# Performance work log

Measured on AMD Instinct MI355X. Metric: run time of the kernel, lower is better.

The kernel has to match this reference:

```python
import jax, jax.numpy as jnp
import numpy as np

D_MODEL = 2048
D_HEAD = 128
NUM_HEADS = 16
D_KV_LATENT = 512
BATCH = 2
SEQ = 2048


def setup_inputs() -> dict:
    key = jax.random.key(0)
    ks = jax.random.split(key, 6)
    s = 0.02
    return {
        "x": jax.random.normal(ks[0], (BATCH, SEQ, D_MODEL), jnp.float32),
        "Wd": jax.random.normal(ks[1], (D_KV_LATENT, D_MODEL), jnp.float32) * s,
        "Wuk": jax.random.normal(ks[2], (NUM_HEADS * D_HEAD, D_KV_LATENT), jnp.float32) * s,
        "Wuv": jax.random.normal(ks[3], (NUM_HEADS * D_HEAD, D_KV_LATENT), jnp.float32) * s,
        "Wq": jax.random.normal(ks[4], (NUM_HEADS * D_HEAD, D_MODEL), jnp.float32) * s,
        "Wo": jax.random.normal(ks[5], (D_MODEL, NUM_HEADS * D_HEAD), jnp.float32) * s,
        "use_cache": 1,
    }


def _mla_cache_path(x, Wd, Wuk, Wuv, Wq, Wo):
    # Weight-absorbed MLA prefill from an empty cache (total_seq_len == seq_len).
    b, s, dm = x.shape
    h, dh, c = NUM_HEADS, D_HEAD, D_KV_LATENT
    # latents = downsample(x): [b, s, c]
    latents = jnp.einsum("bsm,cm->bsc", x, Wd)
    # absorbed weights: q_uk [h, dm, c], out_uv [h, dm, c]
    q_uk = jnp.einsum("hdm,hdc->hmc", Wq.reshape(h, dh, dm), Wuk.reshape(h, dh, c))
    out_uv = jnp.einsum("mhd,hdc->hmc", Wo.reshape(dm, h, dh), Wuv.reshape(h, dh, c))
    # query_part: [b, h, s, c]
    query_part = jnp.einsum("bsm,hmc->bhsc", x, q_uk)
    # value_part: [b, h, s, dm]
    value_part = jnp.einsum("hmc,btc->bhtm", out_uv, latents)
    # scores over latent dim: [b, h, s, s]
    scores = jnp.einsum("bhsc,btc->bhst", query_part, latents) / np.sqrt(dh).astype(np.float32)
    causal = jnp.triu(jnp.ones((s, s), dtype=bool), k=1)
    scores = jnp.where(causal, -jnp.inf, scores)
    attn = jax.nn.softmax(scores, axis=-1)
    # output already in model dim; sum contributions over heads
    out = jnp.einsum("bhst,bhtm->bsm", attn, value_part)
    return out


def reference(x, Wd, Wuk, Wuv, Wq, Wo, use_cache):
    # use_cache is a static Python int (1 -> weight-absorbed cache path)
    return _mla_cache_path(x, Wd, Wuk, Wuv, Wq, Wo)
```

## Files before the change

### kernel.cpp

```cpp
#include <hip/hip_runtime.h>
#include <hip/hip_bf16.h>

typedef __attribute__((ext_vector_type(8))) short short8x;
typedef __attribute__((ext_vector_type(4))) float f32x4;

__device__ __forceinline__ ushort f2bf(float f){
  union { __hip_bfloat16 b; ushort u; } cvt;
  cvt.b = __float2bfloat16(f);
  return cvt.u;
}

__global__ __launch_bounds__(256) void cvt_kernel(const float* __restrict__ in, ushort* __restrict__ out,
                                                  long n, float scale){
  long i = ((long)blockIdx.x * 256 + threadIdx.x) * 4;
  if (i >= n) return;
  float4 v = *(const float4*)(in + i);
  ushort4 o;
  o.x = f2bf(v.x * scale); o.y = f2bf(v.y * scale); o.z = f2bf(v.z * scale); o.w = f2bf(v.w * scale);
  *(ushort4*)(out + i) = o;
}

template<int OUTBF>
__global__ __launch_bounds__(256, 3)
void gemm_bt(const ushort* __restrict__ A, const ushort* __restrict__ BT, void* __restrict__ Cv,
             int M, int N, int K, int lda, int ldb, int ldc,
             long aZ, long bZ, long cZ, float scale)
{
  __shared__ __align__(16) ushort As[2][128 * 32];
  __shared__ __align__(16) ushort Bs[2][128 * 32];
  const int z = blockIdx.z;
  const ushort* Ab = A + (long)z * aZ;
  const ushort* Bb = BT + (long)z * bZ;
  const int tid = threadIdx.x, lane = tid & 63, w = tid >> 6;
  const int wm = w >> 1, wn = w & 1;
  const int lq = lane & 15, q4 = lane >> 4;

  int lin = blockIdx.x + gridDim.x * blockIdx.y;
  const int cpx = (gridDim.x * gridDim.y) >> 3;
  lin = (lin & 7) * cpx + (lin >> 3);
  const int bx = lin % gridDim.x, by = lin / gridDim.x;

  const long arow = (long)by * 128, brow = (long)bx * 128;
  const int lr = lane >> 2, lc = (lane & 3) * 8;

  const f32x4 z4 = {0.f, 0.f, 0.f, 0.f};
  f32x4 acc[4][4];
#pragma unroll
  for (int i = 0; i < 4; i++)
#pragma unroll
    for (int j = 0; j < 4; j++) acc[i][j] = z4;

  auto stage = [&](int buf, int k0){
#pragma unroll
    for (int is = 0; is < 2; ++is){
      const int rb = is * 64 + w * 16;
      const ushort* ga = Ab + (arow + rb + lr) * (long)lda + k0 + lc;
      const ushort* gb = Bb + (brow + rb + lr) * (long)ldb + k0 + lc;
      __builtin_amdgcn_global_load_lds((const __attribute__((address_space(1))) void*)ga,
                                       (__attribute__((address_space(3))) void*)&As[buf][rb * 32], 16, 0, 0);
      __builtin_amdgcn_global_load_lds((const __attribute__((address_space(1))) void*)gb,
                                       (__attribute__((address_space(3))) void*)&Bs[buf][rb * 32], 16, 0, 0);
    }
  };

  const int nk = K >> 5;
  stage(0, 0);
  for (int kt = 0; kt < nk; ++kt){
    __syncthreads();
    if (kt + 1 < nk) stage((kt + 1) & 1, (kt + 1) * 32);
    const int buf = kt & 1;
    short8x a[4], b[4];
#pragma unroll
    for (int i = 0; i < 4; i++){
      a[i] = *(const short8x*)&As[buf][(wm * 64 + i * 16 + lq) * 32 + q4 * 8];
      b[i] = *(const short8x*)&Bs[buf][(wn * 64 + i * 16 + lq) * 32 + q4 * 8];
    }
#pragma unroll
    for (int i = 0; i < 4; i++)
#pragma unroll
      for (int j = 0; j < 4; j++)
        acc[i][j] = __builtin_amdgcn_mfma_f32_16x16x32_bf16(a[i], b[j], acc[i][j], 0, 0, 0);
  }

  const long crowb = arow + wm * 64;
  const long ccolb = brow + wn * 64;
#pragma unroll
  for (int i = 0; i < 4; i++)
#pragma unroll
    for (int j = 0; j < 4; j++)
#pragma unroll
      for (int r = 0; r < 4; r++){
        const long row = crowb + i * 16 + q4 * 4 + r;
        const long col = ccolb + j * 16 + lq;
        const float v = acc[i][j][r] * scale;
        if (OUTBF) ((ushort*)Cv)[(long)z * cZ + row * ldc + col] = f2bf(v);
        else       ((float*)Cv)[(long)z * cZ + row * ldc + col] = v;
      }
}

__global__ __launch_bounds__(256, 1)
void flash12_kernel(const ushort* __restrict__ q, const ushort* __restrict__ k,
                    const ushort* __restrict__ vT, ushort* __restrict__ attnO)
{
  __shared__ __align__(16) ushort Kb[2][64 * 128];
  __shared__ __align__(16) ushort Vb[2][128 * 64];
  __shared__ __align__(16) ushort Pl[4][2][16][64];

  const int tid = threadIdx.x, lane = tid & 63, w = tid >> 6;
  const int lq = lane & 15, q4 = lane >> 4;

  const int i = blockIdx.x;
  const int pr = i >> 8;
  const int ii = i & 255;
  const int xcd = ii & 7;
  const int bh = xcd * 4 + ((ii >> 3) & 3);
  const int j = ii >> 5;
  const int strip = pr ? j : (15 - j);
  const int b = bh & 1, h = bh >> 1;

  const int nt = 2 * (strip + 1);
  const int wdiag = strip * 2 + (w >> 1);
  const int moff = (w & 1) * 32;

  const ushort* kb_ = k + (long)b * 2048 * 2048 + h * 128;
  const ushort* vb_ = vT + (long)h * 128 * 4096 + (long)b * 2048;

  const int krow0 = w * 4 + (lane >> 4);
  const int kg = (lane & 15) ^ (krow0 & 7);
  const ushort* kbase = kb_ + (long)krow0 * 2048 + kg * 8;
  const int kofs0 = w * 512;

  const int drow0 = w * 8 + (lane >> 3);
  const int vg = (lane & 7) ^ (drow0 & 7);
  const ushort* vbase = vb_ + (long)drow0 * 4096 + vg * 8;
  const int vofs0 = w * 512;

  auto stage = [&](int buf, int tt){
    const ushort* kp = kbase + (long)tt * 64 * 2048;
    const ushort* vp = vbase + (long)tt * 64;
#pragma unroll
    for (int is = 0; is < 4; ++is){
      __builtin_amdgcn_global_load_lds((const __attribute__((address_space(1))) void*)(kp + (long)is * 16 * 2048),
          (__attribute__((address_space(3))) void*)&Kb[buf][kofs0 + is * 2048], 16, 0, 0);
      __builtin_amdgcn_global_load_lds((const __attribute__((address_space(1))) void*)(vp + (long)is * 32 * 4096),
          (__attribute__((address_space(3))) void*)&Vb[buf][vofs0 + is * 2048], 16, 0, 0);
    }
  };

  const f32x4 z4 = {0.f, 0.f, 0.f, 0.f};

  const int qrow0 = strip * 128 + w * 32;
  const long qgbase = (long)b * 2048 + qrow0;

  short8x qf[2][4];
#pragma unroll
  for (int si = 0; si < 2; si++){
    const ushort* qp = q + (qgbase + si * 16 + lq) * 2560 + h * 128 + q4 * 8;
#pragma unroll
    for (int ks = 0; ks < 4; ks++) qf[si][ks] = *(const short8x*)(qp + ks * 32);
  }

  f32x4 oacc[8][2];
#pragma unroll
  for (int dt = 0; dt < 8; dt++){ oacc[dt][0] = z4; oacc[dt][1] = z4; }
  float dsum[2] = {0.f, 0.f};

  const int prx = lq & 7;

  stage(0, 0);
  stage(1, 1);

#pragma unroll 1
  for (int tt = 0; tt < nt; ++tt){
    if (tt == nt - 1) asm volatile("s_waitcnt vmcnt(0)" ::: "memory");
    else              asm volatile("s_waitcnt vmcnt(8)" ::: "memory");
    __syncthreads();
    const int cur = tt & 1;

    if (tt <= wdiag){
      const bool diag = (tt == wdiag);
#pragma unroll
      for (int ti = 0; ti < 4; ++ti){
        const int r = ti * 16 + lq;
        const int rb = r * 128;
        const int rx = r & 7;
        const short8x a0 = *(const short8x*)&Kb[cur][rb + (((q4) ^ rx) * 8)];
        const short8x a1 = *(const short8x*)&Kb[cur][rb + (((4 + q4) ^ rx) * 8)];
        const short8x a2 = *(const short8x*)&Kb[cur][rb + (((8 + q4) ^ rx) * 8)];
        const short8x a3 = *(const short8x*)&Kb[cur][rb + (((12 + q4) ^ rx) * 8)];
        const int cG = (ti * 2 + (q4 >> 1)) ^ prx;
        const int pco = cG * 8 + (q4 & 1) * 4;
#pragma unroll
        for (int si = 0; si < 2; ++si){
          f32x4 st = __builtin_amdgcn_mfma_f32_16x16x32_bf16(a0, qf[si][0], z4, 0, 0, 0);
          st = __builtin_amdgcn_mfma_f32_16x16x32_bf16(a1, qf[si][1], st, 0, 0, 0);
          st = __builtin_amdgcn_mfma_f32_16x16x32_bf16(a2, qf[si][2], st, 0, 0, 0);
          st = __builtin_amdgcn_mfma_f32_16x16x32_bf16(a3, qf[si][3], st, 0, 0, 0);
          ushort4 pb;
#pragma unroll
          for (int r4 = 0; r4 < 4; ++r4){
            const int tl = ti * 16 + q4 * 4 + r4;
            float p = exp2f(st[r4]);
            if (diag && tl > moff + si * 16 + lq) p = 0.f;
            dsum[si] += p;
            ((ushort*)&pb)[r4] = f2bf(p);
          }
          *(ushort4*)&Pl[w][si][lq][pco] = pb;
        }
      }
      asm volatile("s_waitcnt lgkmcnt(0)" ::: "memory");
      __builtin_amdgcn_sched_barrier(0);
      const short8x pf00 = *(const short8x*)&Pl[w][0][lq][(q4 ^ prx) * 8];
      const short8x pf01 = *(const short8x*)&Pl[w][0][lq][((4 + q4) ^ prx) * 8];
      const short8x pf10 = *(const short8x*)&Pl[w][1][lq][(q4 ^ prx) * 8];
      const short8x pf11 = *(const short8x*)&Pl[w][1][lq][((4 + q4) ^ prx) * 8];
      __builtin_amdgcn_sched_barrier(0);
#pragma unroll
      for (int dt = 0; dt < 8; ++dt){
        const int r = dt * 16 + lq;
        const int rb = r * 64;
        const int rx = lq & 7;
        const short8x av0 = *(const short8x*)&Vb[cur][rb + (((q4) ^ rx) * 8)];
        const short8x av1 = *(const short8x*)&Vb[cur][rb + (((4 + q4) ^ rx) * 8)];
        oacc[dt][0] = __builtin_amdgcn_mfma_f32_16x16x32_bf16(av0, pf00, oacc[dt][0], 0, 0, 0);
        oacc[dt][0] = __builtin_amdgcn_mfma_f32_16x16x32_bf16(av1, pf01, oacc[dt][0], 0, 0, 0);
        oacc[dt][1] = __builtin_amdgcn_mfma_f32_16x16x32_bf16(av0, pf10, oacc[dt][1], 0, 0, 0);
        oacc[dt][1] = __builtin_amdgcn_mfma_f32_16x16x32_bf16(av1, pf11, oacc[dt][1], 0, 0, 0);
      }
    }
    __syncthreads();
    if (tt + 2 < nt) stage(cur, tt + 2);
  }

  float inv[2];
#pragma unroll
  for (int si = 0; si < 2; ++si){
    float d = dsum[si];
    d += __shfl_xor(d, 16);
    d += __shfl_xor(d, 32);
    inv[si] = 1.f / d;
  }

#pragma unroll
  for (int dt = 0; dt < 8; dt++)
#pragma unroll
    for (int si = 0; si < 2; si++){
      ushort4 o;
      o.x = f2bf(oacc[dt][si][0] * inv[si]);
      o.y = f2bf(oacc[dt][si][1] * inv[si]);
      o.z = f2bf(oacc[dt][si][2] * inv[si]);
      o.w = f2bf(oacc[dt][si][3] * inv[si]);
      *(ushort4*)(attnO + (qgbase + si * 16 + lq) * 2048 + h * 128 + dt * 16 + q4 * 4) = o;
    }
}

extern "C" void kernel_launch(void* const* d_in, const int* in_sizes, int n_in,
                              void* d_out, int out_size, void* d_ws, size_t ws_size,
                              hipStream_t stream)
{
  const float* x   = (const float*)d_in[0];
  const float* Wd  = (const float*)d_in[1];
  const float* Wuk = (const float*)d_in[2];
  const float* Wuv = (const float*)d_in[3];
  const float* Wq  = (const float*)d_in[4];
  const float* Wo  = (const float*)d_in[5];
  float* out = (float*)d_out;
  ushort* ws = (ushort*)d_ws;

  ushort* xb    = ws + 0L;
  ushort* wqdb  = ws + 8388608L;
  ushort* wob   = ws + 13631488L;
  ushort* wukb  = ws + 17825792L;
  ushort* wuvb  = ws + 18874368L;
  ushort* qlat  = ws + 19922944L;
  ushort* kb    = ws + 30408704L;
  ushort* vTb   = ws + 38797312L;
  ushort* attnO = ws + 47185920L;

  const float QSCL = 0.12751744800f;

  cvt_kernel<<<8192, 256, 0, stream>>>(x,   xb,            8388608L, 1.0f);
  cvt_kernel<<<4096, 256, 0, stream>>>(Wq,  wqdb,          4194304L, QSCL);
  cvt_kernel<<<1024, 256, 0, stream>>>(Wd,  wqdb + 4194304L, 1048576L, 1.0f);
  cvt_kernel<<<4096, 256, 0, stream>>>(Wo,  wob,           4194304L, 1.0f);
  cvt_kernel<<<1024, 256, 0, stream>>>(Wuk, wukb,          1048576L, 1.0f);
  cvt_kernel<<<1024, 256, 0, stream>>>(Wuv, wuvb,          1048576L, 1.0f);

  gemm_bt<1><<<dim3(20, 32, 1), 256, 0, stream>>>(xb, wqdb, qlat, 4096, 2560, 2048,
      2048, 2048, 2560, 0L, 0L, 0L, 1.0f);
  gemm_bt<1><<<dim3(16, 32, 1), 256, 0, stream>>>(qlat + 2048, wukb, kb, 4096, 2048, 512,
      2560, 512, 2048, 0L, 0L, 0L, 1.0f);
  gemm_bt<1><<<dim3(32, 16, 1), 256, 0, stream>>>(wuvb, qlat + 2048, vTb, 2048, 4096, 512,
      512, 2560, 4096, 0L, 0L, 0L, 1.0f);
  flash12_kernel<<<512, 256, 0, stream>>>(qlat, kb, vTb, attnO);
  gemm_bt<0><<<dim3(16, 32, 1), 256, 0, stream>>>(attnO, wob, out, 4096, 2048, 2048,
      2048, 2048, 2048, 0L, 0L, 0L, 1.0f);
}
```

Before: 237.8 us.

## Merge conversion kernels, deepen GEMM prefetch, and shrink flash attention tiles

Merges the six fp32-to-bf16 conversion launches into one kernel that picks its source by index range, which removes launch overhead. The GEMM now prefetches two K-tiles ahead, waits on an explicit vmcnt and allows 4 blocks per CU. The attention kernel moves to 128-thread blocks with 64-row query strips and 32-key tiles, doubling the grid to 1024 blocks for better load balance and occupancy. The P buffer drops its swizzle in favour of padding, and the V reads use a new swizzle. Smaller tiles raise sync and stage overhead per unit of work, and the higher GEMM occupancy may cause register spills.

```diff
diff --git a/kernel.cpp b/kernel.cpp
--- a/kernel.cpp
+++ b/kernel.cpp
@@ -10,18 +10,26 @@
   return cvt.u;
 }
 
-__global__ __launch_bounds__(256) void cvt_kernel(const float* __restrict__ in, ushort* __restrict__ out,
-                                                  long n, float scale){
-  long i = ((long)blockIdx.x * 256 + threadIdx.x) * 4;
-  if (i >= n) return;
-  float4 v = *(const float4*)(in + i);
+__global__ __launch_bounds__(256)
+void cvt_all(const float* __restrict__ x, const float* __restrict__ Wq, const float* __restrict__ Wd,
+             const float* __restrict__ Wo, const float* __restrict__ Wuk, const float* __restrict__ Wuv,
+             ushort* __restrict__ out, float qscl){
+  const long i = ((long)blockIdx.x * 256 + threadIdx.x) * 4;
+  const float* src; long off; float scale = 1.0f;
+  if      (i < 8388608L)  { src = x;   off = 0L; }
+  else if (i < 12582912L) { src = Wq;  off = 8388608L;  scale = qscl; }
+  else if (i < 13631488L) { src = Wd;  off = 12582912L; }
+  else if (i < 17825792L) { src = Wo;  off = 13631488L; }
+  else if (i < 18874368L) { src = Wuk; off = 17825792L; }
+  else                    { src = Wuv; off = 18874368L; }
+  const float4 v = *(const float4*)(src + (i - off));
   ushort4 o;
   o.x = f2bf(v.x * scale); o.y = f2bf(v.y * scale); o.z = f2bf(v.z * scale); o.w = f2bf(v.w * scale);
   *(ushort4*)(out + i) = o;
 }
 
 template<int OUTBF>
-__global__ __launch_bounds__(256, 3)
+__global__ __launch_bounds__(256, 4)
 void gemm_bt(const ushort* __restrict__ A, const ushort* __restrict__ BT, void* __restrict__ Cv,
              int M, int N, int K, int lda, int ldb, int ldc,
              long aZ, long bZ, long cZ, float scale)
@@ -50,7 +58,8 @@
 #pragma unroll
     for (int j = 0; j < 4; j++) acc[i][j] = z4;
 
-  auto stage = [&](int buf, int k0){
+  auto stage = [&](int buf, int kt){
+    const int k0 = kt * 32;
 #pragma unroll
     for (int is = 0; is < 2; ++is){
       const int rb = is * 64 + w * 16;
@@ -65,9 +74,12 @@
 
   const int nk = K >> 5;
   stage(0, 0);
+  stage(1, 1);
+#pragma unroll 1
   for (int kt = 0; kt < nk; ++kt){
-    __syncthreads();
-    if (kt + 1 < nk) stage((kt + 1) & 1, (kt + 1) * 32);
+    if (kt == nk - 1) asm volatile("s_waitcnt vmcnt(0)" ::: "memory");
+    else              asm volatile("s_waitcnt vmcnt(4)" ::: "memory");
+    __syncthreads();
     const int buf = kt & 1;
     short8x a[4], b[4];
 #pragma unroll
@@ -80,6 +92,8 @@
 #pragma unroll
       for (int j = 0; j < 4; j++)
         acc[i][j] = __builtin_amdgcn_mfma_f32_16x16x32_bf16(a[i], b[j], acc[i][j], 0, 0, 0);
+    __syncthreads();
+    if (kt + 2 < nk) stage(buf, kt + 2);
   }
 
   const long crowb = arow + wm * 64;
@@ -98,29 +112,26 @@
       }
 }
 
-__global__ __launch_bounds__(256, 1)
-void flash12_kernel(const ushort* __restrict__ q, const ushort* __restrict__ k,
+__global__ __launch_bounds__(128, 2)
+void flash16_kernel(const ushort* __restrict__ q, const ushort* __restrict__ k,
                     const ushort* __restrict__ vT, ushort* __restrict__ attnO)
 {
-  __shared__ __align__(16) ushort Kb[2][64 * 128];
-  __shared__ __align__(16) ushort Vb[2][128 * 64];
-  __shared__ __align__(16) ushort Pl[4][2][16][64];
+  __shared__ __align__(16) ushort Kb[2][32 * 128];
+  __shared__ __align__(16) ushort Vb[2][128 * 32];
+  __shared__ __align__(16) ushort Pl[2][2][16][40];
 
   const int tid = threadIdx.x, lane = tid & 63, w = tid >> 6;
   const int lq = lane & 15, q4 = lane >> 4;
 
-  const int i = blockIdx.x;
-  const int pr = i >> 8;
-  const int ii = i & 255;
-  const int xcd = ii & 7;
-  const int bh = xcd * 4 + ((ii >> 3) & 3);
-  const int j = ii >> 5;
-  const int strip = pr ? j : (15 - j);
+  const int blk = blockIdx.x;
+  const int bh = (blk & 7) * 4 + ((blk >> 3) & 3);
+  const int g = blk >> 5;
+  const int u = (g & 7) * 4 + (g >> 3);
+  const int strip = (u & 1) ? (u >> 1) : (31 - (u >> 1));
   const int b = bh & 1, h = bh >> 1;
 
-  const int nt = 2 * (strip + 1);
-  const int wdiag = strip * 2 + (w >> 1);
-  const int moff = (w & 1) * 32;
+  const int nt = 2 * strip + 2;
+  const int wdiag = 2 * strip + w;
 
   const ushort* kb_ = k + (long)b * 2048 * 2048 + h * 128;
   const ushort* vb_ = vT + (long)h * 128 * 4096 + (long)b * 2048;
@@ -128,28 +139,25 @@
   const int krow0 = w * 4 + (lane >> 4);
   const int kg = (lane & 15) ^ (krow0 & 7);
   const ushort* kbase = kb_ + (long)krow0 * 2048 + kg * 8;
-  const int kofs0 = w * 512;
-
-  const int drow0 = w * 8 + (lane >> 3);
-  const int vg = (lane & 7) ^ (drow0 & 7);
+  const int drow0 = w * 16 + (lane >> 2);
+  const int vg = (lane & 3) ^ ((lane >> 3) & 3);
   const ushort* vbase = vb_ + (long)drow0 * 4096 + vg * 8;
-  const int vofs0 = w * 512;
 
   auto stage = [&](int buf, int tt){
-    const ushort* kp = kbase + (long)tt * 64 * 2048;
-    const ushort* vp = vbase + (long)tt * 64;
+    const ushort* kp = kbase + (long)tt * 32 * 2048;
+    const ushort* vp = vbase + (long)tt * 32;
 #pragma unroll
     for (int is = 0; is < 4; ++is){
-      __builtin_amdgcn_global_load_lds((const __attribute__((address_space(1))) void*)(kp + (long)is * 16 * 2048),
-          (__attribute__((address_space(3))) void*)&Kb[buf][kofs0 + is * 2048], 16, 0, 0);
+      __builtin_amdgcn_global_load_lds((const __attribute__((address_space(1))) void*)(kp + (long)is * 8 * 2048),
+          (__attribute__((address_space(3))) void*)&Kb[buf][is * 1024 + w * 512], 16, 0, 0);
       __builtin_amdgcn_global_load_lds((const __attribute__((address_space(1))) void*)(vp + (long)is * 32 * 4096),
-          (__attribute__((address_space(3))) void*)&Vb[buf][vofs0 + is * 2048], 16, 0, 0);
+          (__attribute__((address_space(3))) void*)&Vb[buf][is * 1024 + w * 512], 16, 0, 0);
     }
   };
 
   const f32x4 z4 = {0.f, 0.f, 0.f, 0.f};
 
-  const int qrow0 = strip * 128 + w * 32;
+  const int qrow0 = strip * 64 + w * 32;
   const long qgbase = (long)b * 2048 + qrow0;
 
   short8x qf[2][4];
@@ -165,7 +173,7 @@
   for (int dt = 0; dt < 8; dt++){ oacc[dt][0] = z4; oacc[dt][1] = z4; }
   float dsum[2] = {0.f, 0.f};
 
-  const int prx = lq & 7;
+  const int rxv = (lq >> 1) & 3;
 
   stage(0, 0);
   stage(1, 1);
@@ -180,16 +188,14 @@
     if (tt <= wdiag){
       const bool diag = (tt == wdiag);
 #pragma unroll
-      for (int ti = 0; ti < 4; ++ti){
+      for (int ti = 0; ti < 2; ++ti){
         const int r = ti * 16 + lq;
         const int rb = r * 128;
-        const int rx = r & 7;
+        const int rx = lq & 7;
         const short8x a0 = *(const short8x*)&Kb[cur][rb + (((q4) ^ rx) * 8)];
         const short8x a1 = *(const short8x*)&Kb[cur][rb + (((4 + q4) ^ rx) * 8)];
         const short8x a2 = *(const short8x*)&Kb[cur][rb + (((8 + q4) ^ rx) * 8)];
         const short8x a3 = *(const short8x*)&Kb[cur][rb + (((12 + q4) ^ rx) * 8)];
-        const int cG = (ti * 2 + (q4 >> 1)) ^ prx;
-        const int pco = cG * 8 + (q4 & 1) * 4;
 #pragma unroll
         for (int si = 0; si < 2; ++si){
           f32x4 st = __builtin_amdgcn_mfma_f32_16x16x32_bf16(a0, qf[si][0], z4, 0, 0, 0);
@@ -201,31 +207,23 @@
           for (int r4 = 0; r4 < 4; ++r4){
             const int tl = ti * 16 + q4 * 4 + r4;
             float p = exp2f(st[r4]);
-            if (diag && tl > moff + si * 16 + lq) p = 0.f;
+            if (diag && tl > si * 16 + lq) p = 0.f;
             dsum[si] += p;
             ((ushort*)&pb)[r4] = f2bf(p);
           }
-          *(ushort4*)&Pl[w][si][lq][pco] = pb;
+          *(ushort4*)&Pl[w][si][lq][ti * 16 + q4 * 4] = pb;
         }
       }
       asm volatile("s_waitcnt lgkmcnt(0)" ::: "memory");
       __builtin_amdgcn_sched_barrier(0);
-      const short8x pf00 = *(const short8x*)&Pl[w][0][lq][(q4 ^ prx) * 8];
-      const short8x pf01 = *(const short8x*)&Pl[w][0][lq][((4 + q4) ^ prx) * 8];
-      const short8x pf10 = *(const short8x*)&Pl[w][1][lq][(q4 ^ prx) * 8];
-      const short8x pf11 = *(const short8x*)&Pl[w][1][lq][((4 + q4) ^ prx) * 8];
+      const short8x pf0 = *(const short8x*)&Pl[w][0][lq][q4 * 8];
+      const short8x pf1 = *(const short8x*)&Pl[w][1][lq][q4 * 8];
       __builtin_amdgcn_sched_barrier(0);
 #pragma unroll
       for (int dt = 0; dt < 8; ++dt){
-        const int r = dt * 16 + lq;
-        const int rb = r * 64;
-        const int rx = lq & 7;
-        const short8x av0 = *(const short8x*)&Vb[cur][rb + (((q4) ^ rx) * 8)];
-        const short8x av1 = *(const short8x*)&Vb[cur][rb + (((4 + q4) ^ rx) * 8)];
-        oacc[dt][0] = __builtin_amdgcn_mfma_f32_16x16x32_bf16(av0, pf00, oacc[dt][0], 0, 0, 0);
-        oacc[dt][0] = __builtin_amdgcn_mfma_f32_16x16x32_bf16(av1, pf01, oacc[dt][0], 0, 0, 0);
-        oacc[dt][1] = __builtin_amdgcn_mfma_f32_16x16x32_bf16(av0, pf10, oacc[dt][1], 0, 0, 0);
-        oacc[dt][1] = __builtin_amdgcn_mfma_f32_16x16x32_bf16(av1, pf11, oacc[dt][1], 0, 0, 0);
+        const short8x av = *(const short8x*)&Vb[cur][(dt * 16 + lq) * 32 + ((q4 ^ rxv) * 8)];
+        oacc[dt][0] = __builtin_amdgcn_mfma_f32_16x16x32_bf16(av, pf0, oacc[dt][0], 0, 0, 0);
+        oacc[dt][1] = __builtin_amdgcn_mfma_f32_16x16x32_bf16(av, pf1, oacc[dt][1], 0, 0, 0);
       }
     }
     __syncthreads();
@@ -279,12 +277,7 @@
 
   const float QSCL = 0.12751744800f;
 
-  cvt_kernel<<<8192, 256, 0, stream>>>(x,   xb,            8388608L, 1.0f);
-  cvt_kernel<<<4096, 256, 0, stream>>>(Wq,  wqdb,          4194304L, QSCL);
-  cvt_kernel<<<1024, 256, 0, stream>>>(Wd,  wqdb + 4194304L, 1048576L, 1.0f);
-  cvt_kernel<<<4096, 256, 0, stream>>>(Wo,  wob,           4194304L, 1.0f);
-  cvt_kernel<<<1024, 256, 0, stream>>>(Wuk, wukb,          1048576L, 1.0f);
-  cvt_kernel<<<1024, 256, 0, stream>>>(Wuv, wuvb,          1048576L, 1.0f);
+  cvt_all<<<19456, 256, 0, stream>>>(x, Wq, Wd, Wo, Wuk, Wuv, ws, QSCL);
 
   gemm_bt<1><<<dim3(20, 32, 1), 256, 0, stream>>>(xb, wqdb, qlat, 4096, 2560, 2048,
       2048, 2048, 2560, 0L, 0L, 0L, 1.0f);
@@ -292,7 +285,7 @@
       2560, 512, 2048, 0L, 0L, 0L, 1.0f);
   gemm_bt<1><<<dim3(32, 16, 1), 256, 0, stream>>>(wuvb, qlat + 2048, vTb, 2048, 4096, 512,
       512, 2560, 4096, 0L, 0L, 0L, 1.0f);
-  flash12_kernel<<<512, 256, 0, stream>>>(qlat, kb, vTb, attnO);
+  flash16_kernel<<<1024, 128, 0, stream>>>(qlat, kb, vTb, attnO);
   gemm_bt<0><<<dim3(16, 32, 1), 256, 0, stream>>>(attnO, wob, out, 4096, 2048, 2048,
       2048, 2048, 2048, 0L, 0L, 0L, 1.0f);
 }
```

New measurement: 238.0 us. Within noise of the previous version (+0.1%).
